# Kernel optimization log

Hardware: AMD Instinct MI355X
Metric: run time of the kernel (lower is better)

## Reference

```python
import jax, jax.numpy as jnp
import numpy as np

EPS = 1e-5


def _conv(x, w, groups=1, pad=0):
    return jax.lax.conv_general_dilated(
        x, w, (1, 1), [(pad, pad), (pad, pad)],
        dimension_numbers=('NCHW', 'OIHW', 'NCHW'),
        feature_group_count=groups)


def _bn(x, p):
    # p: (4, C) rows = gamma, beta, running_mean, running_var (inference BN)
    g, b, m, v = p[0], p[1], p[2], p[3]
    scale = g / jnp.sqrt(v + EPS)
    return (x - m[None, :, None, None]) * scale[None, :, None, None] + b[None, :, None, None]


def _pixel_shuffle(x, r):
    B, C, H, W = x.shape
    x = x.reshape(B, C // (r * r), r, r, H, W)
    x = x.transpose(0, 1, 4, 2, 5, 3)
    return x.reshape(B, C // (r * r), H * r, W * r)


def _grid_sample_border(img, grid):
    # img: (N, C, H, W); grid: (N, Ho, Wo, 2) with (x, y) in [-1, 1]
    # bilinear, align_corners=False, padding_mode='border' (torch semantics)
    N, C, H, W = img.shape
    x = ((grid[..., 0] + 1.0) * W - 1.0) * 0.5
    y = ((grid[..., 1] + 1.0) * H - 1.0) * 0.5
    x = jnp.clip(x, 0.0, W - 1.0)
    y = jnp.clip(y, 0.0, H - 1.0)
    x0 = jnp.floor(x)
    y0 = jnp.floor(y)
    wx = (x - x0)[:, None]  # (N,1,Ho,Wo)
    wy = (y - y0)[:, None]
    x0i = jnp.clip(x0.astype(jnp.int32), 0, W - 1)
    y0i = jnp.clip(y0.astype(jnp.int32), 0, H - 1)
    x1i = jnp.minimum(x0i + 1, W - 1)
    y1i = jnp.minimum(y0i + 1, H - 1)
    gather = jax.vmap(lambda im, yy, xx: im[:, yy, xx])
    v00 = gather(img, y0i, x0i)
    v01 = gather(img, y0i, x1i)
    v10 = gather(img, y1i, x0i)
    v11 = gather(img, y1i, x1i)
    return (v00 * (1 - wy) * (1 - wx) + v01 * (1 - wy) * wx
            + v10 * wy * (1 - wx) + v11 * wy * wx)


def _init_pos(scale, groups, dtype):
    h = jnp.arange((-scale + 1) / 2, (scale - 1) / 2 + 1, dtype=dtype) / scale
    g1, g2 = jnp.meshgrid(h, h, indexing='ij')
    p = jnp.swapaxes(jnp.stack([g1, g2]), 1, 2)  # (2, s, s)
    p = jnp.tile(p, (1, groups, 1))
    return p.reshape(1, -1, 1, 1)  # (1, 2*groups*s*s, 1, 1)


def _dysample(x, ow, ob, scale=2, groups=4):
    # DySample 'lp' style, dyscope=False
    B, C, H, W = x.shape
    off = _conv(x, ow) + ob.reshape(1, -1, 1, 1)
    offset = off * 0.25 + _init_pos(scale, groups, x.dtype)  # (B, 2*g*s^2, H, W)
    offset = offset.reshape(B, 2, -1, H, W)
    cw = jnp.arange(W, dtype=x.dtype) + 0.5
    ch = jnp.arange(H, dtype=x.dtype) + 0.5
    gx, gy = jnp.meshgrid(cw, ch, indexing='ij')  # (W, H)
    coords = jnp.swapaxes(jnp.stack([gx, gy]), 1, 2)[None, :, None]  # (1,2,1,H,W)
    norm = jnp.array([W, H], dtype=x.dtype).reshape(1, 2, 1, 1, 1)
    coords = 2.0 * (coords + offset) / norm - 1.0  # (B,2,g*s^2,H,W)
    coords = _pixel_shuffle(coords.reshape(B, -1, H, W), scale)  # (B, 2*g, sH, sW)
    coords = coords.reshape(B, 2, groups, scale * H, scale * W)
    coords = coords.transpose(0, 2, 3, 4, 1).reshape(B * groups, scale * H, scale * W, 2)
    xs = x.reshape(B * groups, C // groups, H, W)
    out = _grid_sample_border(xs, coords)
    return out.reshape(B, C, scale * H, scale * W)


def _make_bn(key, C):
    k1, k2, k3, k4 = jax.random.split(key, 4)
    gamma = jax.random.uniform(k1, (C,), minval=0.5, maxval=1.5)
    beta = 0.1 * jax.random.normal(k2, (C,))
    mean = 0.1 * jax.random.normal(k3, (C,))
    var = jax.random.uniform(k4, (C,), minval=0.5, maxval=1.5)
    return jnp.stack([gamma, beta, mean, var])


def setup_inputs() -> dict:
    key = jax.random.key(0)
    ks = jax.random.split(key, 24)
    B, C, H, W = 4, 768, 32, 32
    F = 256
    d = {}
    for i in range(4):
        d[f'f{i+1}'] = jax.random.normal(ks[i], (B, C, H, W), dtype=jnp.float32)
    d['proj_w'] = jax.random.normal(ks[4], (4, C, F), dtype=jnp.float32) * (C ** -0.5)
    d['layer_weights'] = jax.random.normal(ks[5], (4,), dtype=jnp.float32)
    d['dw_w'] = jax.random.normal(ks[6], (F, 1, 3, 3), dtype=jnp.float32) * (1.0 / 3.0)
    d['bn_enh'] = _make_bn(ks[7], F)
    cstd = (F * 9) ** -0.5
    d['offset_w1'] = jax.random.normal(ks[8], (32, F, 1, 1), dtype=jnp.float32) * 0.001
    d['offset_b1'] = jnp.zeros((32,), dtype=jnp.float32)
    d['conv_w1'] = jax.random.normal(ks[9], (F, F, 3, 3), dtype=jnp.float32) * cstd
    d['bn1'] = _make_bn(ks[10], F)
    d['offset_w2'] = jax.random.normal(ks[11], (32, F, 1, 1), dtype=jnp.float32) * 0.001
    d['offset_b2'] = jnp.zeros((32,), dtype=jnp.float32)
    d['conv_w2'] = jax.random.normal(ks[12], (F, F, 3, 3), dtype=jnp.float32) * cstd
    d['bn2'] = _make_bn(ks[13], F)
    d['out_w'] = jax.random.normal(ks[14], (1, F, 3, 3), dtype=jnp.float32) * cstd
    d['out_b'] = jnp.zeros((1,), dtype=jnp.float32)
    return d


def reference(f1, f2, f3, f4, proj_w, layer_weights, dw_w, bn_enh,
              offset_w1, offset_b1, conv_w1, bn1,
              offset_w2, offset_b2, conv_w2, bn2, out_w, out_b):
    # --- WeightedFusion: project each layer's tokens, softmax-weighted sum ---
    feats = jnp.stack([f1, f2, f3, f4])  # (L, B, C, H, W)
    L, B, C, H, W = feats.shape
    tokens = feats.reshape(L, B, C, H * W).transpose(0, 1, 3, 2)  # (L, B, N, C)
    proj = jax.nn.gelu(jnp.einsum('lbnc,lcf->lbnf', tokens, proj_w), approximate=False)
    lw = jax.nn.softmax(layer_weights)
    fused = jnp.einsum('l,lbnf->bnf', lw, proj)  # (B, N, 256)
    x = fused.transpose(0, 2, 1).reshape(B, -1, H, W)  # (B, 256, H, W)

    # --- SpatialDetailEnhancer: depthwise conv + BN, residual ReLU ---
    Fc = x.shape[1]
    y = _conv(x, dw_w, groups=Fc, pad=1)
    x = jax.nn.relu(_bn(y, bn_enh) + x)

    x = _dysample(x, offset_w1, offset_b1)
    x = jax.nn.relu(_bn(_conv(x, conv_w1, pad=1), bn1))
    x = _dysample(x, offset_w2, offset_b2)
    x = jax.nn.relu(_bn(_conv(x, conv_w2, pad=1), bn2))

    # --- depth prediction head ---
    out = _conv(x, out_w, pad=1) + out_b.reshape(1, -1, 1, 1)
    return out  # (B, 1, 4H, 4W)
```

## Files before the change

### kernel.cpp

```cpp
#include <hip/hip_runtime.h>
#include <math.h>

using u16 = unsigned short;
typedef __attribute__((ext_vector_type(8))) short short8;
typedef __attribute__((ext_vector_type(4))) float f32x4;

__device__ __forceinline__ float b2f(u16 u) {
    union { unsigned int i; float f; } v; v.i = ((unsigned int)u) << 16; return v.f;
}
__device__ __forceinline__ u16 f2b(float f) {
    union { float f; unsigned int i; } v; v.f = f;
    unsigned int x = v.i;
    return (u16)((x + 0x7FFFu + ((x >> 16) & 1u)) >> 16);
}
__device__ __forceinline__ float ldx(const void* p, long long i, int fl) {
    return fl ? ((const float*)p)[i] : b2f(((const u16*)p)[i]);
}

__global__ __launch_bounds__(256) void k_detect(const void* p, int* flag) {
    __shared__ float m[256];
    int t = threadIdx.x;
    const u16* q = (const u16*)p;
    float lm = 0.f;
    for (int j = 0; j < 16; ++j) {
        float v = b2f(q[t * 16 + j]);
        float a = fabsf(v);
        if (!(a <= 1e30f)) a = 1e31f;
        lm = fmaxf(lm, a);
    }
    m[t] = lm;
    __syncthreads();
    if (t == 0) {
        float mm = 0.f;
        for (int i = 0; i < 256; ++i) mm = fmaxf(mm, m[i]);
        *flag = (mm > 1000.f) ? 1 : 0;
    }
}

__global__ __launch_bounds__(256) void k_wt(const void* __restrict__ w,
                                            u16* __restrict__ wTo,
                                            const int* __restrict__ flag) {
    int fl = *flag;
    int idx = blockIdx.x * 256 + threadIdx.x;
    int k  = idx >> 16;
    int oc = (idx >> 8) & 255;
    int ic = idx & 255;
    long long s = (oc * 256 + ic) * 9 + k;
    wTo[idx] = fl ? f2b(((const float*)w)[s]) : ((const u16*)w)[s];
}

__global__ __launch_bounds__(256) void k_pwt(const void* __restrict__ w,
                                             u16* __restrict__ pwT,
                                             const int* __restrict__ flag) {
    int fl = *flag;
    int idx = blockIdx.x * 256 + threadIdx.x;
    int c = idx % 768;
    int f = (idx / 768) & 255;
    int l = idx / (768 * 256);
    long long s = ((long long)l * 768 + c) * 256 + f;
    pwT[idx] = fl ? f2b(((const float*)w)[s]) : ((const u16*)w)[s];
}

__global__ __launch_bounds__(256) void k_fgemm(
    const void* __restrict__ f1, const void* __restrict__ f2,
    const void* __restrict__ f3, const void* __restrict__ f4,
    const u16* __restrict__ pwT, const void* __restrict__ lwp,
    const int* __restrict__ flag, float* __restrict__ gbuf)
{
    __shared__ u16 As[128][40];
    __shared__ u16 Bs[128][40];
    const int fl = *flag;
    const int t    = threadIdx.x;
    const int lane = t & 63;
    const int wv   = t >> 6;
    const int mbase = (wv & 1) << 6;
    const int nbase = (wv >> 1) << 6;
    const int quad  = lane >> 4;
    const int l15   = lane & 15;

    const int f0 = blockIdx.x << 7;
    const int m0 = blockIdx.y << 7;
    const int b  = blockIdx.z >> 2;
    const int l  = blockIdx.z & 3;
    const void* fp = (l == 0) ? f1 : (l == 1) ? f2 : (l == 2) ? f3 : f4;

    float w0 = ldx(lwp, 0, fl), w1 = ldx(lwp, 1, fl);
    float w2 = ldx(lwp, 2, fl), w3 = ldx(lwp, 3, fl);
    float mx = fmaxf(fmaxf(w0, w1), fmaxf(w2, w3));
    float e0 = expf(w0 - mx), e1 = expf(w1 - mx), e2 = expf(w2 - mx), e3 = expf(w3 - mx);
    float es = e0 + e1 + e2 + e3;
    float lwl = ((l == 0) ? e0 : (l == 1) ? e1 : (l == 2) ? e2 : e3) / es;

    const int spx = t & 127;
    const int sq  = t >> 7;

    f32x4 acc[4][4];
    #pragma unroll
    for (int i = 0; i < 4; ++i)
        #pragma unroll
        for (int j = 0; j < 4; ++j) acc[i][j] = (f32x4)0.f;

    const size_t abase = (size_t)b * 768 * 1024 + m0 + spx;
    const u16* srcB = pwT + (size_t)l * 196608 + (size_t)(f0 + spx) * 768 + sq * 16;

    for (int k0 = 0; k0 < 768; k0 += 32) {
        alignas(16) u16 av[16];
        if (fl) {
            #pragma unroll
            for (int s = 0; s < 16; ++s)
                av[s] = f2b(((const float*)fp)[abase + (size_t)(k0 + sq * 16 + s) * 1024]);
        } else {
            #pragma unroll
            for (int s = 0; s < 16; ++s)
                av[s] = ((const u16*)fp)[abase + (size_t)(k0 + sq * 16 + s) * 1024];
        }
        uint4 bq0 = *(const uint4*)(srcB + k0);
        uint4 bq1 = *(const uint4*)(srcB + k0 + 8);
        __syncthreads();
        *(uint4*)&As[spx][sq * 16]     = *(const uint4*)&av[0];
        *(uint4*)&As[spx][sq * 16 + 8] = *(const uint4*)&av[8];
        *(uint4*)&Bs[spx][sq * 16]     = bq0;
        *(uint4*)&Bs[spx][sq * 16 + 8] = bq1;
        __syncthreads();

        short8 af[4], bf[4];
        #pragma unroll
        for (int i = 0; i < 4; ++i)
            af[i] = *(const short8*)&As[mbase + (i << 4) + l15][quad << 3];
        #pragma unroll
        for (int j = 0; j < 4; ++j)
            bf[j] = *(const short8*)&Bs[nbase + (j << 4) + l15][quad << 3];
        #pragma unroll
        for (int i = 0; i < 4; ++i)
            #pragma unroll
            for (int j = 0; j < 4; ++j)
                acc[i][j] = __builtin_amdgcn_mfma_f32_16x16x32_bf16(
                    af[i], bf[j], acc[i][j], 0, 0, 0);
    }

    #pragma unroll
    for (int j = 0; j < 4; ++j) {
        const int n = f0 + nbase + (j << 4) + l15;
        float* op = gbuf + ((size_t)((l << 2) + b) * 256 + n) * 1024
                  + m0 + mbase + (quad << 2);
        #pragma unroll
        for (int i = 0; i < 4; ++i) {
            f32x4 a = acc[i][j];
            float4 o;
            o.x = lwl * 0.5f * a[0] * (1.f + erff(a[0] * 0.70710678118654752f));
            o.y = lwl * 0.5f * a[1] * (1.f + erff(a[1] * 0.70710678118654752f));
            o.z = lwl * 0.5f * a[2] * (1.f + erff(a[2] * 0.70710678118654752f));
            o.w = lwl * 0.5f * a[3] * (1.f + erff(a[3] * 0.70710678118654752f));
            *(float4*)(op + (i << 4)) = o;
        }
    }
}

__global__ __launch_bounds__(256) void k_fsum(const float* __restrict__ gbuf,
                                              float* __restrict__ x0)
{
    int idx = blockIdx.x * 256 + threadIdx.x;
    x0[idx] = gbuf[idx] + gbuf[1048576 + idx]
            + gbuf[2097152 + idx] + gbuf[3145728 + idx];
}

__global__ __launch_bounds__(256) void k_dw(const float* __restrict__ x0,
                                            const void* __restrict__ dww,
                                            const void* __restrict__ bnp,
                                            const int* __restrict__ flag,
                                            float* __restrict__ x1)
{
    const int fl = *flag;
    int idx = blockIdx.x * 256 + threadIdx.x;
    int n = idx & 1023;
    int f = (idx >> 10) & 255;
    int h = n >> 5, w = n & 31;
    const float* base = x0 + (idx - n);
    float acc = 0.f;
    #pragma unroll
    for (int kh = 0; kh < 3; ++kh) {
        int y = h + kh - 1;
        if (y < 0 || y >= 32) continue;
        #pragma unroll
        for (int kw = 0; kw < 3; ++kw) {
            int x = w + kw - 1;
            if (x < 0 || x >= 32) continue;
            acc += base[(y << 5) + x] * ldx(dww, f * 9 + kh * 3 + kw, fl);
        }
    }
    float g  = ldx(bnp, f, fl);
    float be = ldx(bnp, 256 + f, fl);
    float mn = ldx(bnp, 512 + f, fl);
    float vv = ldx(bnp, 768 + f, fl);
    float scale = g / sqrtf(vv + 1e-5f);
    float o = (acc - mn) * scale + be + x0[idx];
    x1[idx] = fmaxf(o, 0.f);
}

template<bool ACT_BF16>
__global__ __launch_bounds__(256) void k_offs(const void* __restrict__ actv,
                                              const void* __restrict__ w,
                                              const void* __restrict__ bias,
                                              const int* __restrict__ flag,
                                              float* __restrict__ off,
                                              int HW)
{
    const int fl = *flag;
    int idx = blockIdx.x * 256 + threadIdx.x;
    int pos = idx % HW;
    int oc  = (idx / HW) & 31;
    int b   = idx / (32 * HW);
    float acc = 0.f;
    if (ACT_BF16) {
        const u16* ap = (const u16*)actv + (size_t)b * 256 * HW + pos;
        for (int ic = 0; ic < 256; ++ic)
            acc = fmaf(b2f(ap[(size_t)ic * HW]), ldx(w, oc * 256 + ic, fl), acc);
    } else {
        const float* ap = (const float*)actv + (size_t)b * 256 * HW + pos;
        for (int ic = 0; ic < 256; ++ic)
            acc = fmaf(ap[(size_t)ic * HW], ldx(w, oc * 256 + ic, fl), acc);
    }
    off[idx] = acc + ldx(bias, oc, fl);
}

template<bool ACT_BF16>
__global__ __launch_bounds__(256) void k_sample(const void* __restrict__ actv,
                                                const float* __restrict__ off,
                                                u16* __restrict__ out,
                                                int H, int W)
{
    const int Wo = W << 1, Ho = H << 1;
    const int HW = H * W, HWo = Ho * Wo;
    int idx = blockIdx.x * 256 + threadIdx.x;
    int wo = idx % Wo;
    int ho = (idx / Wo) % Ho;
    int c  = (idx / HWo) & 255;
    int b  = idx / (256 * HWo);
    int g  = c >> 6;
    int h = ho >> 1, a = ho & 1, w = wo >> 1, bb = wo & 1;
    int och = g * 4 + a * 2 + bb;
    size_t obase = ((size_t)b * 32 + och) * HW + h * W + w;
    float offx = off[obase];
    float offy = off[obase + (size_t)16 * HW];
    float xp = (float)w + (bb ? 0.25f : -0.25f) + 0.25f * offx;
    float yp = (float)h + (a  ? 0.25f : -0.25f) + 0.25f * offy;
    xp = fminf(fmaxf(xp, 0.f), (float)(W - 1));
    yp = fminf(fmaxf(yp, 0.f), (float)(H - 1));
    float xf = floorf(xp), yf = floorf(yp);
    float wx = xp - xf, wy = yp - yf;
    int x0i = (int)xf; x0i = max(0, min(x0i, W - 1));
    int y0i = (int)yf; y0i = max(0, min(y0i, H - 1));
    int x1i = min(x0i + 1, W - 1);
    int y1i = min(y0i + 1, H - 1);
    float v00, v01, v10, v11;
    if (ACT_BF16) {
        const u16* ap = (const u16*)actv + ((size_t)b * 256 + c) * HW;
        v00 = b2f(ap[y0i * W + x0i]);
        v01 = b2f(ap[y0i * W + x1i]);
        v10 = b2f(ap[y1i * W + x0i]);
        v11 = b2f(ap[y1i * W + x1i]);
    } else {
        const float* ap = (const float*)actv + ((size_t)b * 256 + c) * HW;
        v00 = ap[y0i * W + x0i];
        v01 = ap[y0i * W + x1i];
        v10 = ap[y1i * W + x0i];
        v11 = ap[y1i * W + x1i];
    }
    float r = v00 * (1.f - wy) * (1.f - wx) + v01 * (1.f - wy) * wx
            + v10 * wy * (1.f - wx) + v11 * wy * wx;
    out[idx] = f2b(r);
}

__global__ __launch_bounds__(256) void k_cmfma(const u16* __restrict__ in,
                                               const u16* __restrict__ wTo,
                                               const void* __restrict__ bnp,
                                               const int* __restrict__ flag,
                                               u16* __restrict__ out,
                                               int H, int W, int logW)
{
    __shared__ u16 As[128][40];
    __shared__ u16 Bs[128][40];
    const int fl = *flag;
    const int HW = H * W;
    const int t    = threadIdx.x;
    const int lane = t & 63;
    const int wv   = t >> 6;
    const int mbase = (wv & 1) << 6;
    const int nbase = (wv >> 1) << 6;
    const int quad  = lane >> 4;
    const int l15   = lane & 15;

    const int oc0 = blockIdx.x << 7;
    const int px0 = blockIdx.y << 7;
    const u16* inb  = in  + (size_t)blockIdx.z * 256 * HW;
    u16*       outb = out + (size_t)blockIdx.z * 256 * HW;

    const int spx = t & 127;
    const int sq  = t >> 7;
    const int gx = (px0 + spx) & (W - 1);
    const int gy = (px0 + spx) >> logW;

    f32x4 acc[4][4];
    #pragma unroll
    for (int i = 0; i < 4; ++i)
        #pragma unroll
        for (int j = 0; j < 4; ++j) acc[i][j] = (f32x4)0.f;

    for (int k3 = 0; k3 < 9; ++k3) {
        const int dh = k3 / 3, dw = k3 % 3;
        const int ys = gy + dh - 1;
        const int xs = gx + dw - 1;
        const bool valid = (ys >= 0) && (ys < H) && (xs >= 0) && (xs < W);
        const u16* srcA = inb + (size_t)(sq * 16) * HW + ys * W + xs;
        const u16* srcB = wTo + (size_t)k3 * 65536 + (size_t)(oc0 + spx) * 256 + sq * 16;

        for (int ic0 = 0; ic0 < 256; ic0 += 32) {
            alignas(16) u16 av[16];
            if (valid) {
                #pragma unroll
                for (int s = 0; s < 16; ++s)
                    av[s] = srcA[(size_t)(ic0 + s) * HW];
            } else {
                #pragma unroll
                for (int s = 0; s < 16; ++s) av[s] = 0;
            }
            uint4 bq0 = *(const uint4*)(srcB + ic0);
            uint4 bq1 = *(const uint4*)(srcB + ic0 + 8);
            __syncthreads();
            *(uint4*)&As[spx][sq * 16]     = *(const uint4*)&av[0];
            *(uint4*)&As[spx][sq * 16 + 8] = *(const uint4*)&av[8];
            *(uint4*)&Bs[spx][sq * 16]     = bq0;
            *(uint4*)&Bs[spx][sq * 16 + 8] = bq1;
            __syncthreads();

            short8 af[4], bf[4];
            #pragma unroll
            for (int i = 0; i < 4; ++i)
                af[i] = *(const short8*)&As[mbase + (i << 4) + l15][quad << 3];
            #pragma unroll
            for (int j = 0; j < 4; ++j)
                bf[j] = *(const short8*)&Bs[nbase + (j << 4) + l15][quad << 3];
            #pragma unroll
            for (int i = 0; i < 4; ++i)
                #pragma unroll
                for (int j = 0; j < 4; ++j)
                    acc[i][j] = __builtin_amdgcn_mfma_f32_16x16x32_bf16(
                        af[i], bf[j], acc[i][j], 0, 0, 0);
        }
    }

    #pragma unroll
    for (int j = 0; j < 4; ++j) {
        const int n = oc0 + nbase + (j << 4) + l15;
        float g  = ldx(bnp, n, fl);
        float be = ldx(bnp, 256 + n, fl);
        float mn = ldx(bnp, 512 + n, fl);
        float vv = ldx(bnp, 768 + n, fl);
        float scale = g / sqrtf(vv + 1e-5f);
        u16* op = outb + (size_t)n * HW + px0 + mbase + (quad << 2);
        #pragma unroll
        for (int i = 0; i < 4; ++i) {
            f32x4 a = acc[i][j];
            ushort4 o;
            o.x = f2b(fmaxf((a[0] - mn) * scale + be, 0.f));
            o.y = f2b(fmaxf((a[1] - mn) * scale + be, 0.f));
            o.z = f2b(fmaxf((a[2] - mn) * scale + be, 0.f));
            o.w = f2b(fmaxf((a[3] - mn) * scale + be, 0.f));
            *(ushort4*)(op + (i << 4)) = o;
        }
    }
}

__global__ __launch_bounds__(256) void k_headp(const u16* __restrict__ in,
                                               const void* __restrict__ w,
                                               const int* __restrict__ flag,
                                               float* __restrict__ part)
{
    const int fl = *flag;
    const int icc = blockIdx.x;
    const int px  = blockIdx.y * 256 + threadIdx.x;
    in   += (size_t)blockIdx.z * 256 * 16384;
    part += (size_t)blockIdx.z * 16 * 16384;
    const int x = px & 127, y = px >> 7;
    float acc = 0.f;
    #pragma unroll 4
    for (int i = 0; i < 16; ++i) {
        const int ic = (icc << 4) + i;
        const u16* p = in + (size_t)ic * 16384;
        float wr[9];
        #pragma unroll
        for (int k = 0; k < 9; ++k) wr[k] = ldx(w, ic * 9 + k, fl);
        #pragma unroll
        for (int kh = 0; kh < 3; ++kh) {
            int yy = y + kh - 1;
            if (yy < 0 || yy >= 128) continue;
            const u16* row = p + yy * 128;
            #pragma unroll
            for (int kw = 0; kw < 3; ++kw) {
                int xx = x + kw - 1;
                if (xx < 0 || xx >= 128) continue;
                acc = fmaf(b2f(row[xx]), wr[kh * 3 + kw], acc);
            }
        }
    }
    part[icc * 16384 + px] = acc;
}

__global__ __launch_bounds__(256) void k_headf(const float* __restrict__ part,
                                               const void* __restrict__ bias,
                                               const int* __restrict__ flag,
                                               void* __restrict__ outp,
                                               int b0)
{
    const int fl = *flag;
    int px = blockIdx.x * 256 + threadIdx.x;
    part += (size_t)blockIdx.y * 16 * 16384;
    int out_ofs = (b0 + blockIdx.y) * 16384;
    float acc = ldx(bias, 0, fl);
    #pragma unroll
    for (int i = 0; i < 16; ++i) acc += part[i * 16384 + px];
    if (fl) ((float*)outp)[out_ofs + px] = acc;
    else    ((u16*)outp)[out_ofs + px] = f2b(acc);
}

extern "C" void kernel_launch(void* const* d_in, const int* in_sizes, int n_in,
                              void* d_out, int out_size, void* d_ws, size_t ws_size,
                              hipStream_t stream) {
    (void)in_sizes; (void)n_in; (void)out_size;
    const void* f1     = d_in[0];
    const void* f2     = d_in[1];
    const void* f3     = d_in[2];
    const void* f4     = d_in[3];
    const void* proj_w = d_in[4];
    const void* lwp    = d_in[5];
    const void* dw_w   = d_in[6];
    const void* bn_enh = d_in[7];
    const void* ow1    = d_in[8];
    const void* ob1    = d_in[9];
    const void* cw1    = d_in[10];
    const void* bn1    = d_in[11];
    const void* ow2    = d_in[12];
    const void* ob2    = d_in[13];
    const void* cw2    = d_in[14];
    const void* bn2    = d_in[15];
    const void* out_w  = d_in[16];
    const void* out_b  = d_in[17];

    const int nb = (ws_size >= 81592320ull) ? 4
                 : (ws_size >= 48037888ull) ? 2 : 1;

    char* ws = (char*)d_ws;
    int*   flag = (int*)  (ws + 0);
    u16*   wT1  = (u16*)  (ws + 65536);
    u16*   wT2  = (u16*)  (ws + 1245184);
    u16*   pwT  = (u16*)  (ws + 2424832);
    u16*   c1   = (u16*)  (ws + 3997696);
    float* o2   = (float*)(ws + 12386304);
    u16*   up2c = (u16*)  (ws + 14483456);
    u16*   c2c  = (u16*)  (ws + 14483456 + (size_t)nb * 8388608);
    float* part = (float*)(ws + 14483456);
    float* gbuf = (float*)(ws + 3997696);
    float* x0   = (float*)(ws + 20774912);
    float* x1   = (float*)(ws + 24969216);
    float* o1   = (float*)(ws + 29163520);
    u16*   up1  = (u16*)  (ws + 12386304);

    k_detect<<<1, 256, 0, stream>>>(f1, flag);

    k_wt<<<2304, 256, 0, stream>>>(cw1, wT1, flag);
    k_wt<<<2304, 256, 0, stream>>>(cw2, wT2, flag);
    k_pwt<<<3072, 256, 0, stream>>>(proj_w, pwT, flag);

    k_fgemm<<<dim3(2, 8, 16), 256, 0, stream>>>(f1, f2, f3, f4, pwT, lwp, flag, gbuf);
    k_fsum<<<4096, 256, 0, stream>>>(gbuf, x0);

    k_dw<<<4096, 256, 0, stream>>>(x0, dw_w, bn_enh, flag, x1);

    k_offs<false><<<512, 256, 0, stream>>>(x1, ow1, ob1, flag, o1, 32 * 32);
    k_sample<false><<<16384, 256, 0, stream>>>(x1, o1, up1, 32, 32);
    k_cmfma<<<dim3(2, 32, 4), 256, 0, stream>>>(up1, wT1, bn1, flag, c1, 64, 64, 6);

    k_offs<true><<<2048, 256, 0, stream>>>(c1, ow2, ob2, flag, o2, 64 * 64);

    for (int b0 = 0; b0 < 4; b0 += nb) {
        const u16*   c1b = c1 + (size_t)b0 * 256 * 4096;
        const float* o2b = o2 + (size_t)b0 * 32 * 4096;
        k_sample<true><<<16384 * nb, 256, 0, stream>>>(c1b, o2b, up2c, 64, 64);
        k_cmfma<<<dim3(2, 128, nb), 256, 0, stream>>>(up2c, wT2, bn2, flag, c2c,
                                                      128, 128, 7);
        k_headp<<<dim3(16, 64, nb), 256, 0, stream>>>(c2c, out_w, flag, part);
        k_headf<<<dim3(64, nb), 256, 0, stream>>>(part, out_b, flag, d_out, b0);
    }
}
```

Before: 645.4 us.

## Double-buffer LDS tiles in fused GEMM and conv MFMA kernels

```diff
diff --git a/kernel.cpp b/kernel.cpp
--- a/kernel.cpp
+++ b/kernel.cpp
@@ -61,14 +61,58 @@
     pwT[idx] = fl ? f2b(((const float*)w)[s]) : ((const u16*)w)[s];
 }
 
+__device__ __forceinline__ void st32(u16 (*A)[40], u16 (*B)[40],
+                                     int spx, int sq,
+                                     const u16* av, const uint4* bq) {
+    *(uint4*)&A[spx][sq * 16]     = ((const uint4*)av)[0];
+    *(uint4*)&A[spx][sq * 16 + 8] = ((const uint4*)av)[1];
+    *(uint4*)&B[spx][sq * 16]     = bq[0];
+    *(uint4*)&B[spx][sq * 16 + 8] = bq[1];
+}
+
+__device__ __forceinline__ void mfma32(const u16 (*A)[40], const u16 (*B)[40],
+                                       int mbase, int nbase, int l15, int quad,
+                                       f32x4 acc[4][4]) {
+    short8 af[4], bf[4];
+    #pragma unroll
+    for (int i = 0; i < 4; ++i)
+        af[i] = *(const short8*)&A[mbase + (i << 4) + l15][quad << 3];
+    #pragma unroll
+    for (int j = 0; j < 4; ++j)
+        bf[j] = *(const short8*)&B[nbase + (j << 4) + l15][quad << 3];
+    #pragma unroll
+    for (int i = 0; i < 4; ++i)
+        #pragma unroll
+        for (int j = 0; j < 4; ++j)
+            acc[i][j] = __builtin_amdgcn_mfma_f32_16x16x32_bf16(
+                af[i], bf[j], acc[i][j], 0, 0, 0);
+}
+
+__device__ __forceinline__ void fg_gather(const void* fp, const u16* pwB, int fl,
+                                          size_t abase, int s, int sq,
+                                          u16* av, uint4* bq) {
+    const int k0 = s * 32;
+    if (fl) {
+        const float* src = (const float*)fp + abase + (size_t)(k0 + sq * 16) * 1024;
+        #pragma unroll
+        for (int i = 0; i < 16; ++i) av[i] = f2b(src[(size_t)i * 1024]);
+    } else {
+        const u16* src = (const u16*)fp + abase + (size_t)(k0 + sq * 16) * 1024;
+        #pragma unroll
+        for (int i = 0; i < 16; ++i) av[i] = src[(size_t)i * 1024];
+    }
+    bq[0] = *(const uint4*)(pwB + k0);
+    bq[1] = *(const uint4*)(pwB + k0 + 8);
+}
+
 __global__ __launch_bounds__(256) void k_fgemm(
     const void* __restrict__ f1, const void* __restrict__ f2,
     const void* __restrict__ f3, const void* __restrict__ f4,
     const u16* __restrict__ pwT, const void* __restrict__ lwp,
     const int* __restrict__ flag, float* __restrict__ gbuf)
 {
-    __shared__ u16 As[128][40];
-    __shared__ u16 Bs[128][40];
+    __shared__ u16 As[2][128][40];
+    __shared__ u16 Bs[2][128][40];
     const int fl = *flag;
     const int t    = threadIdx.x;
     const int lane = t & 63;
@@ -93,6 +137,8 @@
 
     const int spx = t & 127;
     const int sq  = t >> 7;
+    const size_t abase = (size_t)b * 768 * 1024 + m0 + spx;
+    const u16* pwB = pwT + (size_t)l * 196608 + (size_t)(f0 + spx) * 768 + sq * 16;
 
     f32x4 acc[4][4];
     #pragma unroll
@@ -100,42 +146,23 @@
         #pragma unroll
         for (int j = 0; j < 4; ++j) acc[i][j] = (f32x4)0.f;
 
-    const size_t abase = (size_t)b * 768 * 1024 + m0 + spx;
-    const u16* srcB = pwT + (size_t)l * 196608 + (size_t)(f0 + spx) * 768 + sq * 16;
-
-    for (int k0 = 0; k0 < 768; k0 += 32) {
-        alignas(16) u16 av[16];
-        if (fl) {
-            #pragma unroll
-            for (int s = 0; s < 16; ++s)
-                av[s] = f2b(((const float*)fp)[abase + (size_t)(k0 + sq * 16 + s) * 1024]);
-        } else {
-            #pragma unroll
-            for (int s = 0; s < 16; ++s)
-                av[s] = ((const u16*)fp)[abase + (size_t)(k0 + sq * 16 + s) * 1024];
+    alignas(16) u16 av[16];
+    uint4 bq[2];
+    const int NS = 24;
+    fg_gather(fp, pwB, fl, abase, 0, sq, av, bq);
+    st32(As[0], Bs[0], spx, sq, av, bq);
+    __syncthreads();
+    for (int s = 0; s < NS; s += 2) {
+        fg_gather(fp, pwB, fl, abase, s + 1, sq, av, bq);
+        mfma32(As[0], Bs[0], mbase, nbase, l15, quad, acc);
+        st32(As[1], Bs[1], spx, sq, av, bq);
+        __syncthreads();
+        if (s + 2 < NS) fg_gather(fp, pwB, fl, abase, s + 2, sq, av, bq);
+        mfma32(As[1], Bs[1], mbase, nbase, l15, quad, acc);
+        if (s + 2 < NS) {
+            st32(As[0], Bs[0], spx, sq, av, bq);
+            __syncthreads();
         }
-        uint4 bq0 = *(const uint4*)(srcB + k0);
-        uint4 bq1 = *(const uint4*)(srcB + k0 + 8);
-        __syncthreads();
-        *(uint4*)&As[spx][sq * 16]     = *(const uint4*)&av[0];
-        *(uint4*)&As[spx][sq * 16 + 8] = *(const uint4*)&av[8];
-        *(uint4*)&Bs[spx][sq * 16]     = bq0;
-        *(uint4*)&Bs[spx][sq * 16 + 8] = bq1;
-        __syncthreads();
-
-        short8 af[4], bf[4];
-        #pragma unroll
-        for (int i = 0; i < 4; ++i)
-            af[i] = *(const short8*)&As[mbase + (i << 4) + l15][quad << 3];
-        #pragma unroll
-        for (int j = 0; j < 4; ++j)
-            bf[j] = *(const short8*)&Bs[nbase + (j << 4) + l15][quad << 3];
-        #pragma unroll
-        for (int i = 0; i < 4; ++i)
-            #pragma unroll
-            for (int j = 0; j < 4; ++j)
-                acc[i][j] = __builtin_amdgcn_mfma_f32_16x16x32_bf16(
-                    af[i], bf[j], acc[i][j], 0, 0, 0);
     }
 
     #pragma unroll
@@ -271,6 +298,29 @@
     out[idx] = f2b(r);
 }
 
+__device__ __forceinline__ void cm_gather(const u16* inb, const u16* wTo,
+                                          int s, int sq, int gx, int gy,
+                                          int H, int W, int HW, int oc0, int spx,
+                                          u16* av, uint4* bq) {
+    const int k3  = s >> 3;
+    const int ic0 = (s & 7) << 5;
+    const int dh = k3 / 3, dw = k3 - dh * 3;
+    const int ys = gy + dh - 1, xs = gx + dw - 1;
+    const bool valid = (ys >= 0) && (ys < H) && (xs >= 0) && (xs < W);
+    const u16* pA = inb + (size_t)(ic0 + sq * 16) * HW + ys * W + xs;
+    if (valid) {
+        #pragma unroll
+        for (int i = 0; i < 16; ++i) av[i] = pA[(size_t)i * HW];
+    } else {
+        #pragma unroll
+        for (int i = 0; i < 16; ++i) av[i] = 0;
+    }
+    const u16* pB = wTo + (size_t)k3 * 65536 + (size_t)(oc0 + spx) * 256
+                  + ic0 + sq * 16;
+    bq[0] = *(const uint4*)pB;
+    bq[1] = *(const uint4*)(pB + 8);
+}
+
 __global__ __launch_bounds__(256) void k_cmfma(const u16* __restrict__ in,
                                                const u16* __restrict__ wTo,
                                                const void* __restrict__ bnp,
@@ -278,8 +328,8 @@
                                                u16* __restrict__ out,
                                                int H, int W, int logW)
 {
-    __shared__ u16 As[128][40];
-    __shared__ u16 Bs[128][40];
+    __shared__ u16 As[2][128][40];
+    __shared__ u16 Bs[2][128][40];
     const int fl = *flag;
     const int HW = H * W;
     const int t    = threadIdx.x;
@@ -306,46 +356,23 @@
         #pragma unroll
         for (int j = 0; j < 4; ++j) acc[i][j] = (f32x4)0.f;
 
-    for (int k3 = 0; k3 < 9; ++k3) {
-        const int dh = k3 / 3, dw = k3 % 3;
-        const int ys = gy + dh - 1;
-        const int xs = gx + dw - 1;
-        const bool valid = (ys >= 0) && (ys < H) && (xs >= 0) && (xs < W);
-        const u16* srcA = inb + (size_t)(sq * 16) * HW + ys * W + xs;
-        const u16* srcB = wTo + (size_t)k3 * 65536 + (size_t)(oc0 + spx) * 256 + sq * 16;
-
-        for (int ic0 = 0; ic0 < 256; ic0 += 32) {
-            alignas(16) u16 av[16];
-            if (valid) {
-                #pragma unroll
-                for (int s = 0; s < 16; ++s)
-                    av[s] = srcA[(size_t)(ic0 + s) * HW];
-            } else {
-                #pragma unroll
-                for (int s = 0; s < 16; ++s) av[s] = 0;
-            }
-            uint4 bq0 = *(const uint4*)(srcB + ic0);
-            uint4 bq1 = *(const uint4*)(srcB + ic0 + 8);
+    alignas(16) u16 av[16];
+    uint4 bq[2];
+    const int NS = 72;
+    cm_gather(inb, wTo, 0, sq, gx, gy, H, W, HW, oc0, spx, av, bq);
+    st32(As[0], Bs[0], spx, sq, av, bq);
+    __syncthreads();
+    for (int s = 0; s < NS; s += 2) {
+        cm_gather(inb, wTo, s + 1, sq, gx, gy, H, W, HW, oc0, spx, av, bq);
+        mfma32(As[0], Bs[0], mbase, nbase, l15, quad, acc);
+        st32(As[1], Bs[1], spx, sq, av, bq);
+        __syncthreads();
+        if (s + 2 < NS)
+            cm_gather(inb, wTo, s + 2, sq, gx, gy, H, W, HW, oc0, spx, av, bq);
+        mfma32(As[1], Bs[1], mbase, nbase, l15, quad, acc);
+        if (s + 2 < NS) {
+            st32(As[0], Bs[0], spx, sq, av, bq);
             __syncthreads();
-            *(uint4*)&As[spx][sq * 16]     = *(const uint4*)&av[0];
-            *(uint4*)&As[spx][sq * 16 + 8] = *(const uint4*)&av[8];
-            *(uint4*)&Bs[spx][sq * 16]     = bq0;
-            *(uint4*)&Bs[spx][sq * 16 + 8] = bq1;
-            __syncthreads();
-
-            short8 af[4], bf[4];
-            #pragma unroll
-            for (int i = 0; i < 4; ++i)
-                af[i] = *(const short8*)&As[mbase + (i << 4) + l15][quad << 3];
-            #pragma unroll
-            for (int j = 0; j < 4; ++j)
-                bf[j] = *(const short8*)&Bs[nbase + (j << 4) + l15][quad << 3];
-            #pragma unroll
-            for (int i = 0; i < 4; ++i)
-                #pragma unroll
-                for (int j = 0; j < 4; ++j)
-                    acc[i][j] = __builtin_amdgcn_mfma_f32_16x16x32_bf16(
-                        af[i], bf[j], acc[i][j], 0, 0, 0);
         }
     }
 
```

Measured after the change: 729.0 us. 13.0% more time.

## Write upsampled activations channels-last so conv GEMM loads A with vector reads

Applied to the files above, without the earlier changes.

```diff
diff --git a/kernel.cpp b/kernel.cpp
--- a/kernel.cpp
+++ b/kernel.cpp
@@ -231,14 +231,14 @@
 {
     const int Wo = W << 1, Ho = H << 1;
     const int HW = H * W, HWo = Ho * Wo;
-    int idx = blockIdx.x * 256 + threadIdx.x;
-    int wo = idx % Wo;
-    int ho = (idx / Wo) % Ho;
-    int c  = (idx / HWo) & 255;
-    int b  = idx / (256 * HWo);
-    int g  = c >> 6;
-    int h = ho >> 1, a = ho & 1, w = wo >> 1, bb = wo & 1;
-    int och = g * 4 + a * 2 + bb;
+    const int c   = threadIdx.x;
+    const int pxo = blockIdx.x;
+    const int b   = blockIdx.y;
+    const int wo = pxo % Wo;
+    const int ho = pxo / Wo;
+    const int g  = c >> 6;
+    const int h = ho >> 1, a = ho & 1, w = wo >> 1, bb = wo & 1;
+    const int och = g * 4 + a * 2 + bb;
     size_t obase = ((size_t)b * 32 + och) * HW + h * W + w;
     float offx = off[obase];
     float offy = off[obase + (size_t)16 * HW];
@@ -268,7 +268,7 @@
     }
     float r = v00 * (1.f - wy) * (1.f - wx) + v01 * (1.f - wy) * wx
             + v10 * wy * (1.f - wx) + v11 * wy * wx;
-    out[idx] = f2b(r);
+    out[((size_t)b * HWo + pxo) * 256 + c] = f2b(r);
 }
 
 __global__ __launch_bounds__(256) void k_cmfma(const u16* __restrict__ in,
@@ -311,24 +311,23 @@
         const int ys = gy + dh - 1;
         const int xs = gx + dw - 1;
         const bool valid = (ys >= 0) && (ys < H) && (xs >= 0) && (xs < W);
-        const u16* srcA = inb + (size_t)(sq * 16) * HW + ys * W + xs;
+        const u16* rowA = inb + ((size_t)(ys * W + xs)) * 256 + sq * 16;
         const u16* srcB = wTo + (size_t)k3 * 65536 + (size_t)(oc0 + spx) * 256 + sq * 16;
 
         for (int ic0 = 0; ic0 < 256; ic0 += 32) {
-            alignas(16) u16 av[16];
+            uint4 aq0, aq1;
             if (valid) {
-                #pragma unroll
-                for (int s = 0; s < 16; ++s)
-                    av[s] = srcA[(size_t)(ic0 + s) * HW];
+                aq0 = *(const uint4*)(rowA + ic0);
+                aq1 = *(const uint4*)(rowA + ic0 + 8);
             } else {
-                #pragma unroll
-                for (int s = 0; s < 16; ++s) av[s] = 0;
+                aq0 = make_uint4(0, 0, 0, 0);
+                aq1 = make_uint4(0, 0, 0, 0);
             }
             uint4 bq0 = *(const uint4*)(srcB + ic0);
             uint4 bq1 = *(const uint4*)(srcB + ic0 + 8);
             __syncthreads();
-            *(uint4*)&As[spx][sq * 16]     = *(const uint4*)&av[0];
-            *(uint4*)&As[spx][sq * 16 + 8] = *(const uint4*)&av[8];
+            *(uint4*)&As[spx][sq * 16]     = aq0;
+            *(uint4*)&As[spx][sq * 16 + 8] = aq1;
             *(uint4*)&Bs[spx][sq * 16]     = bq0;
             *(uint4*)&Bs[spx][sq * 16 + 8] = bq1;
             __syncthreads();
@@ -477,7 +476,7 @@
     k_dw<<<4096, 256, 0, stream>>>(x0, dw_w, bn_enh, flag, x1);
 
     k_offs<false><<<512, 256, 0, stream>>>(x1, ow1, ob1, flag, o1, 32 * 32);
-    k_sample<false><<<16384, 256, 0, stream>>>(x1, o1, up1, 32, 32);
+    k_sample<false><<<dim3(4096, 4), 256, 0, stream>>>(x1, o1, up1, 32, 32);
     k_cmfma<<<dim3(2, 32, 4), 256, 0, stream>>>(up1, wT1, bn1, flag, c1, 64, 64, 6);
 
     k_offs<true><<<2048, 256, 0, stream>>>(c1, ow2, ob2, flag, o2, 64 * 64);
@@ -485,7 +484,7 @@
     for (int b0 = 0; b0 < 4; b0 += nb) {
         const u16*   c1b = c1 + (size_t)b0 * 256 * 4096;
         const float* o2b = o2 + (size_t)b0 * 32 * 4096;
-        k_sample<true><<<16384 * nb, 256, 0, stream>>>(c1b, o2b, up2c, 64, 64);
+        k_sample<true><<<dim3(16384, nb), 256, 0, stream>>>(c1b, o2b, up2c, 64, 64);
         k_cmfma<<<dim3(2, 128, nb), 256, 0, stream>>>(up2c, wT2, bn2, flag, c2c,
                                                       128, 128, 7);
         k_headp<<<dim3(16, 64, nb), 256, 0, stream>>>(c2c, out_w, flag, part);
```

After: 752.6 us. 16.6% more time.
